# Kernel tuning notes

Hardware: AMD Instinct MI355X
Metric: run time of the kernel (lower is better)

The kernel has to match this reference:

```python
import jax, jax.numpy as jnp
import numpy as np

NEG = -1.0e4  # neg_limit sentinel used for masked max-pool (fp16-safe)

def setup_inputs() -> dict:
    B, S, H, MW = 4, 2048, 768, 8
    N = S * MW  # num_spans = seq_len * max_span_width
    key = jax.random.key(0)
    k1, k2, k3, k4, k5 = jax.random.split(key, 5)
    token_reps = jax.random.normal(k1, (B, S, H), dtype=jnp.float32)
    starts = jax.random.randint(k2, (B, N), 0, S)
    widths = jax.random.randint(k3, (B, N), 1, MW + 1)
    ends = jnp.minimum(starts + widths, S)  # end-exclusive, <= seq_len
    span_ids = jnp.stack([starts, ends], axis=-1).astype(jnp.int64)
    span_masks = jax.random.uniform(k4, (B, N)) < 0.7
    # ProjectionLayer(2*hidden -> hidden): linear reprojection (dropout inactive at eval)
    W = jax.random.normal(k5, (2 * H, H), dtype=jnp.float32) * 0.02
    b = jnp.zeros((H,), dtype=jnp.float32)
    return {"token_reps": token_reps, "span_ids": span_ids, "span_masks": span_masks,
            "pooling": 0, "W": W, "b": b}

def _window_max(token_reps, idx, valid):
    # idx, valid: (B, N, w); gather tokens then masked max over the window
    B, S, H = token_reps.shape
    w = idx.shape[-1]
    idxc = jnp.clip(idx, 0, S - 1).reshape(B, -1, 1)          # (B, N*w, 1)
    g = jnp.take_along_axis(token_reps, idxc, axis=1)          # (B, N*w, H)
    g = g.reshape(B, -1, w, H)                                 # (B, N, w, H)
    g = jnp.where(valid[..., None], g, NEG)
    return g.max(axis=2)                                       # (B, N, H)

def reference(token_reps, span_ids, span_masks, pooling, W, b):
    # Faithful to extract_span_reps(mode='start_end') but via direct gather+max
    # over the fixed window instead of a (B,N,S,H) broadcasted mask.
    window = 1 if pooling else 3
    starts = span_ids[..., 0]
    ends = span_ids[..., 1]
    offs = jnp.arange(window)
    # start window: [start, min(start+window, end))
    s_idx = starts[..., None] + offs                                   # (B,N,w)
    s_valid = (s_idx < ends[..., None]) & span_masks[..., None]
    # end window: [max(end-window, start), end)
    e_idx = ends[..., None] - window + offs                            # (B,N,w)
    e_valid = (e_idx >= starts[..., None]) & span_masks[..., None]
    start_reps = _window_max(token_reps, s_idx, s_valid)
    end_reps = _window_max(token_reps, e_idx, e_valid)
    span_reps = jnp.concatenate([start_reps, end_reps], axis=-1)       # (B,N,2H)
    span_reps = jnp.where(span_masks[..., None], span_reps, 0.0)
    # out_project: Linear(2H -> H)
    return jnp.einsum('bnd,dh->bnh', span_reps, W) + b
```

## Files before the change

kernel.cpp:

```cpp
#include <hip/hip_runtime.h>
#include <hip/hip_bf16.h>

#define NB 4
#define SEQ 2048
#define HID 768
#define NSPAN 16384
#define M_TOT (NB * NSPAN)
#define K2 1536
#define MROWS (NB * 3 * SEQ)
#define CMP_CAP 66560
#define MT_TOT 520
#define NWG_OLD (MT_TOT * 6)
#define NWG_NEW 2304

typedef float f32x4 __attribute__((ext_vector_type(4)));
typedef short s16x8 __attribute__((ext_vector_type(8)));
typedef unsigned short u16x4 __attribute__((ext_vector_type(4)));
using bf16 = __hip_bfloat16;

__device__ __forceinline__ void gll16(const void* g, void* l) {
    __builtin_amdgcn_global_load_lds(
        (const __attribute__((address_space(1))) unsigned*)g,
        (__attribute__((address_space(3))) unsigned*)l, 16, 0, 0);
}

__device__ __forceinline__ float bf2f(unsigned short v) {
    union { unsigned u; float f; } cv; cv.u = ((unsigned)v) << 16; return cv.f;
}

__global__ void mask_detect_kernel(const unsigned* __restrict__ masks, int* __restrict__ flag) {
    int t = blockIdx.x * 256 + threadIdx.x;
    if (t < 16384) {
        unsigned v = masks[t];
        if (v > 1u) atomicOr(flag, 1);
    }
}

__device__ __forceinline__ bool mask_at(const int* masks, int u8, int m) {
    return u8 ? (((const unsigned char*)masks)[m] != 0) : (masks[m] != 0);
}

__global__ void prep_m3_kernel(const float* __restrict__ T, bf16* __restrict__ M3) {
    int b = blockIdx.y;
    int p0 = blockIdx.x * 16;
    int t = threadIdx.x;
    const float* Tb = T + (size_t)b * SEQ * HID;
    bf16* o0 = M3 + (size_t)(b * 3 + 0) * SEQ * HID;
    bf16* o1 = M3 + (size_t)(b * 3 + 1) * SEQ * HID;
    bf16* o2 = M3 + (size_t)(b * 3 + 2) * SEQ * HID;
#pragma unroll
    for (int c = 0; c < 3; ++c) {
        int h = t + c * 256;
        float x0 = Tb[(size_t)p0 * HID + h];
        float x1 = Tb[(size_t)min(p0 + 1, SEQ - 1) * HID + h];
        for (int i = 0; i < 16; ++i) {
            int p = p0 + i;
            float x2 = Tb[(size_t)min(p + 2, SEQ - 1) * HID + h];
            float m2 = fmaxf(x0, x1);
            float m3v = fmaxf(m2, x2);
            size_t off = (size_t)p * HID + h;
            o0[off] = __float2bfloat16(x0);
            o1[off] = __float2bfloat16(m2);
            o2[off] = __float2bfloat16(m3v);
            x0 = x1; x1 = x2;
        }
    }
}


__global__ void prep_wt2_kernel(const float* __restrict__ W, bf16* __restrict__ Wt) {
    __shared__ float tile[64][65];
    int k0 = blockIdx.x * 64;
    int n0 = blockIdx.y * 64;
    int half = (n0 >= HID) ? 1 : 0;
    int nn = n0 - half * HID;
    int t = threadIdx.x;
    int c = t & 63, r4 = t >> 6;
    for (int r = r4; r < 64; r += 4)
        tile[r][c] = W[(size_t)(half * HID + k0 + r) * HID + nn + c];
    __syncthreads();
    for (int r = r4; r < 64; r += 4)
        Wt[(size_t)(n0 + r) * HID + k0 + c] = __float2bfloat16(tile[c][r]);
}

__global__ __launch_bounds__(256, 4)
void dense_gemm_kernel(const bf16* __restrict__ M3, const bf16* __restrict__ Wt,
                       bf16* __restrict__ P) {
    __shared__ char lA[16384];
    __shared__ char lB[16384];

    const int tid = threadIdx.x;
    const int x = blockIdx.x;
    const int g = x & 7, j = x >> 3;
    const int mt = (j / 12) * 8 + g;
    const int ns = j % 12;
    const int m0 = mt * 128, n0 = ns * 128;

    const int lane = tid & 63, w = tid >> 6;
    const int wr = w >> 1, wc = w & 1;
    const int lr = lane & 15, lg = lane >> 4;
    const int lrow8 = lane >> 3;
    const int chunkp = ((lane & 7) ^ lrow8) << 4;

    const char* aPtr[4];
    const char* bPtr[4];
    int ldsOff[4];
#pragma unroll
    for (int it = 0; it < 4; ++it) {
        int i = it * 4 + w;
        int r = i * 8 + lrow8;
        aPtr[it] = (const char*)M3 + (size_t)(m0 + r) * (HID * 2) + chunkp;
        bPtr[it] = (const char*)Wt + (size_t)(n0 + r) * (HID * 2) + chunkp;
        ldsOff[it] = i * 1024;
    }

    f32x4 acc[4][4];
#pragma unroll
    for (int i = 0; i < 4; i++)
#pragma unroll
        for (int j2 = 0; j2 < 4; j2++) acc[i][j2] = (f32x4){0.f, 0.f, 0.f, 0.f};

    for (int kt = 0; kt < HID; kt += 64) {
        const int colB = kt * 2;
        __syncthreads();
#pragma unroll
        for (int it = 0; it < 4; ++it)
            gll16(aPtr[it] + colB, lA + ldsOff[it]);
#pragma unroll
        for (int it = 0; it < 4; ++it)
            gll16(bPtr[it] + colB, lB + ldsOff[it]);
        __syncthreads();
#pragma unroll
        for (int kk = 0; kk < 2; ++kk) {
            const int cb = kk * 4 + lg;
            s16x8 af[4], bfr[4];
#pragma unroll
            for (int i = 0; i < 4; ++i) {
                int row = wr * 64 + i * 16 + lr;
                af[i] = *(const s16x8*)(lA + row * 128 + ((cb ^ (row & 7)) << 4));
            }
#pragma unroll
            for (int j2 = 0; j2 < 4; ++j2) {
                int row = wc * 64 + j2 * 16 + lr;
                bfr[j2] = *(const s16x8*)(lB + row * 128 + ((cb ^ (row & 7)) << 4));
            }
#pragma unroll
            for (int i = 0; i < 4; ++i)
#pragma unroll
                for (int j2 = 0; j2 < 4; ++j2)
                    acc[i][j2] = __builtin_amdgcn_mfma_f32_16x16x32_bf16(af[i], bfr[j2], acc[i][j2], 0, 0, 0);
        }
    }

    unsigned short* Pu = (unsigned short*)P;
#pragma unroll
    for (int i = 0; i < 4; i++) {
#pragma unroll
        for (int j2 = 0; j2 < 4; j2++) {
#pragma unroll
            for (int q = 0; q < 4; q++) {
                int prow = m0 + wr * 64 + i * 16 + lg * 4 + q;
                int pcol = n0 + wc * 64 + j2 * 16 + lr;
                bf16 v = __float2bfloat16(acc[i][j2][q]);
                Pu[(size_t)prow * K2 + pcol] = *(unsigned short*)&v;
            }
        }
    }
}

__global__ __launch_bounds__(256)
void epilogue_kernel(const bf16* __restrict__ P, const int* __restrict__ span_ids,
                     const int* __restrict__ masks, const int* __restrict__ flag,
                     const int* __restrict__ pooling, const float* __restrict__ bias,
                     float* __restrict__ out) {
    int gw = (blockIdx.x * 256 + threadIdx.x) >> 6;
    int lane = threadIdx.x & 63;
    int u8 = flag[0];
    int window = (pooling[0] != 0) ? 1 : 3;
    const unsigned short* Pu = (const unsigned short*)P;
    for (int m = gw; m < M_TOT; m += 8192) {
        float* orow = out + (size_t)m * HID;
        if (!mask_at(masks, u8, m)) {
#pragma unroll
            for (int rnd = 0; rnd < 3; ++rnd) {
                int n = rnd * 256 + lane * 4;
                *(f32x4*)(orow + n) = *(const f32x4*)(bias + n);
            }
            continue;
        }
        int s = span_ids[2 * m], e = span_ids[2 * m + 1];
        int b = m >> 14;
        int cw = min(window, e - s);
        int base = (b * 3 + (cw - 1)) * SEQ;
        const unsigned short* ps = Pu + (size_t)(base + s) * K2;
        const unsigned short* pe = Pu + (size_t)(base + e - cw) * K2 + HID;
#pragma unroll
        for (int rnd = 0; rnd < 3; ++rnd) {
            int n = rnd * 256 + lane * 4;
            u16x4 a = *(const u16x4*)(ps + n);
            u16x4 c = *(const u16x4*)(pe + n);
            f32x4 bb = *(const f32x4*)(bias + n);
            f32x4 r;
#pragma unroll
            for (int k = 0; k < 4; ++k) r[k] = bf2f(a[k]) + bf2f(c[k]) + bb[k];
            *(f32x4*)(orow + n) = r;
        }
    }
}


__global__ void init_compact_kernel(int* __restrict__ cS, int* __restrict__ cE,
                                    int* __restrict__ cO) {
    int i = blockIdx.x * 256 + threadIdx.x;
    if (i < CMP_CAP) { cS[i] = 0; cE[i] = 0; cO[i] = -1; }
}

__global__ void count_kernel(const int* __restrict__ masks, const int* __restrict__ flag,
                             int* __restrict__ blockCnt) {
    int bid = blockIdx.x, tid = threadIdx.x;
    bool act = mask_at(masks, flag[0], bid * 256 + tid);
    unsigned long long b = __ballot(act);
    __shared__ int wc[4];
    if ((tid & 63) == 0) wc[tid >> 6] = __popcll(b);
    __syncthreads();
    if (tid == 0) blockCnt[bid] = wc[0] + wc[1] + wc[2] + wc[3];
}

__global__ void scan_kernel(const int* __restrict__ blockCnt, int* __restrict__ blockOff,
                            int* __restrict__ cnt) {
    __shared__ int s[256];
    int t = threadIdx.x;
    int mine = blockCnt[t];
    s[t] = mine;
    __syncthreads();
    for (int d = 1; d < 256; d <<= 1) {
        int v = (t >= d) ? s[t - d] : 0;
        __syncthreads();
        s[t] += v;
        __syncthreads();
    }
    blockOff[t] = s[t] - mine;
    if (t == 255) cnt[0] = s[255];
}

__global__ void scatter_kernel(const int* __restrict__ span_ids, const int* __restrict__ masks,
                               const int* __restrict__ flag, const int* __restrict__ pooling,
                               const int* __restrict__ blockOff,
                               int* __restrict__ cS, int* __restrict__ cE,
                               int* __restrict__ cO, int* __restrict__ cI) {
    int bid = blockIdx.x, tid = threadIdx.x;
    int m = bid * 256 + tid;
    bool act = mask_at(masks, flag[0], m);
    unsigned long long b = __ballot(act);
    __shared__ int wA[4], wI[4];
    int lane = tid & 63, w = tid >> 6;
    int wAct = __popcll(b);
    if (lane == 0) { wA[w] = wAct; wI[w] = 64 - wAct; }
    __syncthreads();
    if (tid == 0) {
        int a = 0, ii = 0;
#pragma unroll
        for (int i = 0; i < 4; ++i) {
            int ca = wA[i], ci = wI[i];
            wA[i] = a; wI[i] = ii; a += ca; ii += ci;
        }
    }
    __syncthreads();
    unsigned long long below = (lane == 63) ? ~0ULL >> 1 : ((1ULL << lane) - 1ULL);
    if (act) {
        int rank = __popcll(b & below);
        int idx = blockOff[bid] + wA[w] + rank;
        int s = span_ids[2 * m], e = span_ids[2 * m + 1];
        int bb = m >> 14;
        int window = (pooling[0] != 0) ? 1 : 3;
        int cw = min(window, e - s);
        int base = (bb * 3 + (cw - 1)) * SEQ;
        cS[idx] = base + s;
        cE[idx] = base + (e - cw);
        cO[idx] = m;
    } else {
        int rank = __popcll(~b & below);
        int idx = (bid * 256 - blockOff[bid]) + wI[w] + rank;
        cI[idx] = m;
    }
}

__global__ void prep_wt_old_kernel(const float* __restrict__ W, bf16* __restrict__ Wt) {
    __shared__ float tile[64][65];
    int k0 = blockIdx.x * 64;
    int n0 = blockIdx.y * 64;
    int t = threadIdx.x;
    int c = t & 63, r4 = t >> 6;
    for (int r = r4; r < 64; r += 4)
        tile[r][c] = W[(size_t)(k0 + r) * HID + n0 + c];
    __syncthreads();
    for (int r = r4; r < 64; r += 4)
        Wt[(size_t)(n0 + r) * K2 + k0 + c] = __float2bfloat16(tile[c][r]);
}

__global__ __launch_bounds__(256, 4)
void span_gemm_old_kernel(const bf16* __restrict__ M3, const bf16* __restrict__ Wt,
                          const int* __restrict__ cS, const int* __restrict__ cE,
                          const int* __restrict__ cO, const int* __restrict__ cI,
                          const int* __restrict__ cnt,
                          const float* __restrict__ bias, float* __restrict__ out) {
    __shared__ char lA[128 * 128];
    __shared__ char lB[128 * 128];
    __shared__ int rS[128], rE[128], rO[128];

    const int tid = threadIdx.x;
    const int x = blockIdx.x;
    const int g = x & 7, j = x >> 3;
    const int mt = (j / 6) * 8 + g;
    const int ns = j % 6;
    const int n0 = ns * 128;

    const int count = cnt[0];
    const int actT = (count + 127) >> 7;

    if (mt >= actT) {
        int r = (mt - actT) * 128 + (tid >> 1);
        if (r < M_TOT - count) {
            int o = cI[r];
            const float* bsrc = bias + n0 + (tid & 1) * 64;
            float* dst = out + (size_t)o * HID + n0 + (tid & 1) * 64;
#pragma unroll
            for (int c = 0; c < 16; ++c)
                *(f32x4*)(dst + c * 4) = *(const f32x4*)(bsrc + c * 4);
        }
        return;
    }

    const int m0 = mt * 128;
    if (tid < 128) {
        int m = m0 + tid;
        rS[tid] = cS[m];
        rE[tid] = cE[m];
        rO[tid] = cO[m];
    }
    __syncthreads();

    const int lane = tid & 63, w = tid >> 6;
    const int wr = w >> 1, wc = w & 1;
    const int lr = lane & 15, lg = lane >> 4;
    const int lrow8 = lane >> 3;
    const int chunkp = ((lane & 7) ^ lrow8) << 4;

    const char* aPtr[2][4];
    const char* bPtr[4];
    int ldsOff[4];
#pragma unroll
    for (int it = 0; it < 4; ++it) {
        int i = it * 4 + w;
        int r = i * 8 + lrow8;
        aPtr[0][it] = (const char*)M3 + (size_t)rS[r] * (HID * 2) + chunkp;
        aPtr[1][it] = (const char*)M3 + (size_t)rE[r] * (HID * 2) + chunkp;
        bPtr[it]    = (const char*)Wt + (size_t)(n0 + r) * (K2 * 2) + chunkp;
        ldsOff[it]  = i * 1024;
    }

    f32x4 acc[4][4];
#pragma unroll
    for (int i = 0; i < 4; i++)
#pragma unroll
        for (int j2 = 0; j2 < 4; j2++) acc[i][j2] = (f32x4){0.f, 0.f, 0.f, 0.f};

    for (int kt = 0; kt < K2; kt += 64) {
        const int half = (kt >= HID) ? 1 : 0;
        const int colB = (kt - (half ? HID : 0)) * 2;
        const int ktB  = kt * 2;
        __syncthreads();
#pragma unroll
        for (int it = 0; it < 4; ++it)
            gll16(aPtr[half][it] + colB, lA + ldsOff[it]);
#pragma unroll
        for (int it = 0; it < 4; ++it)
            gll16(bPtr[it] + ktB, lB + ldsOff[it]);
        __syncthreads();
#pragma unroll
        for (int kk = 0; kk < 2; ++kk) {
            const int cb = kk * 4 + lg;
            s16x8 af[4], bfr[4];
#pragma unroll
            for (int i = 0; i < 4; ++i) {
                int row = wr * 64 + i * 16 + lr;
                af[i] = *(const s16x8*)(lA + row * 128 + ((cb ^ (row & 7)) << 4));
            }
#pragma unroll
            for (int j2 = 0; j2 < 4; ++j2) {
                int row = wc * 64 + j2 * 16 + lr;
                bfr[j2] = *(const s16x8*)(lB + row * 128 + ((cb ^ (row & 7)) << 4));
            }
#pragma unroll
            for (int i = 0; i < 4; ++i)
#pragma unroll
                for (int j2 = 0; j2 < 4; ++j2)
                    acc[i][j2] = __builtin_amdgcn_mfma_f32_16x16x32_bf16(af[i], bfr[j2], acc[i][j2], 0, 0, 0);
        }
    }

#pragma unroll
    for (int i = 0; i < 4; i++) {
#pragma unroll
        for (int j2 = 0; j2 < 4; j2++) {
#pragma unroll
            for (int q = 0; q < 4; q++) {
                int mloc = wr * 64 + i * 16 + lg * 4 + q;
                int o = rO[mloc];
                if (o >= 0) {
                    int n = n0 + wc * 64 + j2 * 16 + lr;
                    out[(size_t)o * HID + n] = acc[i][j2][q] + bias[n];
                }
            }
        }
    }
}

extern "C" void kernel_launch(void* const* d_in, const int* in_sizes, int n_in,
                              void* d_out, int out_size, void* d_ws, size_t ws_size,
                              hipStream_t stream) {
    const float* token_reps = (const float*)d_in[0];
    const int*   span_ids   = (const int*)d_in[1];
    const int*   span_masks = (const int*)d_in[2];
    const int*   pooling    = (const int*)d_in[3];
    const float* W          = (const float*)d_in[4];
    const float* bias       = (const float*)d_in[5];
    float* out = (float*)d_out;

    char* ws = (char*)d_ws;
    int*  flag = (int*)ws;

    const size_t M3_OFF   = (size_t)2 << 20;
    const size_t M3_BYTES = (size_t)MROWS * HID * 2;
    bf16* M3 = (bf16*)(ws + M3_OFF);

    const size_t WT2_OFF  = M3_OFF + M3_BYTES;
    const size_t WT2_BYTES = (size_t)K2 * HID * 2;
    const size_t P_OFF    = WT2_OFF + WT2_BYTES;
    const size_t P_BYTES  = (size_t)MROWS * K2 * 2;
    const size_t NEED_NEW = P_OFF + P_BYTES;

    hipMemsetAsync(ws, 0, 64, stream);
    mask_detect_kernel<<<64, 256, 0, stream>>>((const unsigned*)span_masks, flag);
    prep_m3_kernel<<<dim3(SEQ / 16, NB), 256, 0, stream>>>(token_reps, M3);

    if (ws_size >= NEED_NEW) {
        bf16* Wt2 = (bf16*)(ws + WT2_OFF);
        bf16* P   = (bf16*)(ws + P_OFF);
        prep_wt2_kernel<<<dim3(HID / 64, K2 / 64), 256, 0, stream>>>(W, Wt2);
        dense_gemm_kernel<<<NWG_NEW, 256, 0, stream>>>(M3, Wt2, P);
        epilogue_kernel<<<2048, 256, 0, stream>>>(P, span_ids, span_masks, flag,
                                                  pooling, bias, out);
    } else {
        int* cnt      = (int*)(ws + 4);
        int* blockCnt = (int*)(ws + 1024);
        int* blockOff = (int*)(ws + 2048);
        int* cS = (int*)(ws + 4096);
        int* cE = (int*)(ws + 4096 + 4 * (size_t)CMP_CAP);
        int* cO = (int*)(ws + 4096 + 8 * (size_t)CMP_CAP);
        int* cI = (int*)(ws + 4096 + 12 * (size_t)CMP_CAP);
        bf16* WtOld = (bf16*)(ws + WT2_OFF);
        init_compact_kernel<<<(CMP_CAP + 255) / 256, 256, 0, stream>>>(cS, cE, cO);
        count_kernel<<<M_TOT / 256, 256, 0, stream>>>(span_masks, flag, blockCnt);
        scan_kernel<<<1, 256, 0, stream>>>(blockCnt, blockOff, cnt);
        scatter_kernel<<<M_TOT / 256, 256, 0, stream>>>(span_ids, span_masks, flag,
                                                        pooling, blockOff, cS, cE, cO, cI);
        prep_wt_old_kernel<<<dim3(K2 / 64, HID / 64), 256, 0, stream>>>(W, WtOld);
        span_gemm_old_kernel<<<NWG_OLD, 256, 0, stream>>>(
            M3, WtOld, cS, cE, cO, cI, cnt, bias, out);
    }
}
```

Before: 149.7 us.

## Restructure dense GEMM into 256x128 tiles with 512 threads and multi-buffered async LDS pipeline

Measured after the change: 159.9 us. 1.07x slower.

```diff
diff --git a/kernel.cpp b/kernel.cpp
--- a/kernel.cpp
+++ b/kernel.cpp
@@ -8,10 +8,11 @@
 #define M_TOT (NB * NSPAN)
 #define K2 1536
 #define MROWS (NB * 3 * SEQ)
+#define NT12 12
 #define CMP_CAP 66560
 #define MT_TOT 520
 #define NWG_OLD (MT_TOT * 6)
-#define NWG_NEW 2304
+#define NWG_NEW 1152
 
 typedef float f32x4 __attribute__((ext_vector_type(4)));
 typedef short s16x8 __attribute__((ext_vector_type(8)));
@@ -83,36 +84,45 @@
         Wt[(size_t)(n0 + r) * HID + k0 + c] = __float2bfloat16(tile[c][r]);
 }
 
-__global__ __launch_bounds__(256, 4)
+__global__ __launch_bounds__(512, 1)
 void dense_gemm_kernel(const bf16* __restrict__ M3, const bf16* __restrict__ Wt,
                        bf16* __restrict__ P) {
-    __shared__ char lA[16384];
-    __shared__ char lB[16384];
+    __shared__ char lds[131072];
 
     const int tid = threadIdx.x;
     const int x = blockIdx.x;
     const int g = x & 7, j = x >> 3;
     const int mt = (j / 12) * 8 + g;
     const int ns = j % 12;
-    const int m0 = mt * 128, n0 = ns * 128;
+    const int m0 = mt * 256, n0 = ns * 128;
 
     const int lane = tid & 63, w = tid >> 6;
-    const int wr = w >> 1, wc = w & 1;
+    const int wm = w >> 1, wn = w & 1;
     const int lr = lane & 15, lg = lane >> 4;
-    const int lrow8 = lane >> 3;
-    const int chunkp = ((lane & 7) ^ lrow8) << 4;
-
-    const char* aPtr[4];
-    const char* bPtr[4];
-    int ldsOff[4];
-#pragma unroll
-    for (int it = 0; it < 4; ++it) {
-        int i = it * 4 + w;
-        int r = i * 8 + lrow8;
-        aPtr[it] = (const char*)M3 + (size_t)(m0 + r) * (HID * 2) + chunkp;
-        bPtr[it] = (const char*)Wt + (size_t)(n0 + r) * (HID * 2) + chunkp;
-        ldsOff[it] = i * 1024;
-    }
+
+    const int srow_w = w * 8 + (lane >> 3);
+    const int swz = ((lane & 7) ^ ((lane >> 3) & 7)) << 4;
+    const char* aSrc[4];
+    const char* bSrc[2];
+#pragma unroll
+    for (int q = 0; q < 4; ++q)
+        aSrc[q] = (const char*)M3 + (size_t)(m0 + q * 64 + srow_w) * (HID * 2) + swz;
+#pragma unroll
+    for (int q = 0; q < 2; ++q)
+        bSrc[q] = (const char*)Wt + (size_t)(n0 + q * 64 + srow_w) * (HID * 2) + swz;
+    const int dstOff = w * 1024;
+
+#define ST_A(T) do { char* _b = lds + ((T) % 3) * 32768; const int _c = (T) * 128; \
+        gll16(aSrc[0] + _c, _b + 0 * 8192 + dstOff); \
+        gll16(aSrc[1] + _c, _b + 1 * 8192 + dstOff); \
+        gll16(aSrc[2] + _c, _b + 2 * 8192 + dstOff); \
+        gll16(aSrc[3] + _c, _b + 3 * 8192 + dstOff); } while (0)
+#define ST_B(T) do { char* _b = lds + 98304 + ((T) & 1) * 16384; const int _c = (T) * 128; \
+        gll16(bSrc[0] + _c, _b + 0 * 8192 + dstOff); \
+        gll16(bSrc[1] + _c, _b + 1 * 8192 + dstOff); } while (0)
+#define FENCE_BAR() do { __builtin_amdgcn_sched_barrier(0); \
+        __builtin_amdgcn_s_barrier(); \
+        __builtin_amdgcn_sched_barrier(0); } while (0)
 
     f32x4 acc[4][4];
 #pragma unroll
@@ -120,37 +130,69 @@
 #pragma unroll
         for (int j2 = 0; j2 < 4; j2++) acc[i][j2] = (f32x4){0.f, 0.f, 0.f, 0.f};
 
-    for (int kt = 0; kt < HID; kt += 64) {
-        const int colB = kt * 2;
-        __syncthreads();
-#pragma unroll
-        for (int it = 0; it < 4; ++it)
-            gll16(aPtr[it] + colB, lA + ldsOff[it]);
-#pragma unroll
-        for (int it = 0; it < 4; ++it)
-            gll16(bPtr[it] + colB, lB + ldsOff[it]);
-        __syncthreads();
-#pragma unroll
-        for (int kk = 0; kk < 2; ++kk) {
-            const int cb = kk * 4 + lg;
-            s16x8 af[4], bfr[4];
-#pragma unroll
-            for (int i = 0; i < 4; ++i) {
-                int row = wr * 64 + i * 16 + lr;
-                af[i] = *(const s16x8*)(lA + row * 128 + ((cb ^ (row & 7)) << 4));
-            }
-#pragma unroll
-            for (int j2 = 0; j2 < 4; ++j2) {
-                int row = wc * 64 + j2 * 16 + lr;
-                bfr[j2] = *(const s16x8*)(lB + row * 128 + ((cb ^ (row & 7)) << 4));
-            }
-#pragma unroll
-            for (int i = 0; i < 4; ++i)
-#pragma unroll
-                for (int j2 = 0; j2 < 4; ++j2)
-                    acc[i][j2] = __builtin_amdgcn_mfma_f32_16x16x32_bf16(af[i], bfr[j2], acc[i][j2], 0, 0, 0);
-        }
-    }
+    ST_A(0); ST_B(0); ST_A(1); ST_B(1);
+
+    for (int t = 0; t < NT12; ++t) {
+        const char* Ab = lds + (t % 3) * 32768;
+        const char* Bb = lds + 98304 + (t & 1) * 16384;
+        s16x8 bfr[4][2];
+
+        if (t < NT12 - 1) { asm volatile("s_waitcnt vmcnt(6)" ::: "memory"); }
+        else              { asm volatile("s_waitcnt vmcnt(0)" ::: "memory"); }
+        FENCE_BAR();
+        if (t + 2 < NT12) ST_A(t + 2);
+#pragma unroll
+        for (int jf = 0; jf < 4; ++jf) {
+            int row = wn * 64 + jf * 16 + lr;
+#pragma unroll
+            for (int ks = 0; ks < 2; ++ks)
+                bfr[jf][ks] = *(const s16x8*)(Bb + row * 128 + ((((ks << 2) | lg) ^ (row & 7)) << 4));
+        }
+        {
+            s16x8 af[2][2];
+#pragma unroll
+            for (int i = 0; i < 2; ++i) {
+                int row = wm * 64 + i * 16 + lr;
+#pragma unroll
+                for (int ks = 0; ks < 2; ++ks)
+                    af[i][ks] = *(const s16x8*)(Ab + row * 128 + ((((ks << 2) | lg) ^ (row & 7)) << 4));
+            }
+            __builtin_amdgcn_s_setprio(1);
+#pragma unroll
+            for (int ks = 0; ks < 2; ++ks)
+#pragma unroll
+                for (int i = 0; i < 2; ++i)
+#pragma unroll
+                    for (int jf = 0; jf < 4; ++jf)
+                        acc[i][jf] = __builtin_amdgcn_mfma_f32_16x16x32_bf16(af[i][ks], bfr[jf][ks], acc[i][jf], 0, 0, 0);
+            __builtin_amdgcn_s_setprio(0);
+        }
+
+        FENCE_BAR();
+        if (t + 2 < NT12) ST_B(t + 2);
+        {
+            s16x8 af[2][2];
+#pragma unroll
+            for (int i = 0; i < 2; ++i) {
+                int row = wm * 64 + (i + 2) * 16 + lr;
+#pragma unroll
+                for (int ks = 0; ks < 2; ++ks)
+                    af[i][ks] = *(const s16x8*)(Ab + row * 128 + ((((ks << 2) | lg) ^ (row & 7)) << 4));
+            }
+            __builtin_amdgcn_s_setprio(1);
+#pragma unroll
+            for (int ks = 0; ks < 2; ++ks)
+#pragma unroll
+                for (int i = 0; i < 2; ++i)
+#pragma unroll
+                    for (int jf = 0; jf < 4; ++jf)
+                        acc[i + 2][jf] = __builtin_amdgcn_mfma_f32_16x16x32_bf16(af[i][ks], bfr[jf][ks], acc[i + 2][jf], 0, 0, 0);
+            __builtin_amdgcn_s_setprio(0);
+        }
+    }
+#undef ST_A
+#undef ST_B
+#undef FENCE_BAR
 
     unsigned short* Pu = (unsigned short*)P;
 #pragma unroll
@@ -159,8 +201,8 @@
         for (int j2 = 0; j2 < 4; j2++) {
 #pragma unroll
             for (int q = 0; q < 4; q++) {
-                int prow = m0 + wr * 64 + i * 16 + lg * 4 + q;
-                int pcol = n0 + wc * 64 + j2 * 16 + lr;
+                int prow = m0 + wm * 64 + i * 16 + lg * 4 + q;
+                int pcol = n0 + wn * 64 + j2 * 16 + lr;
                 bf16 v = __float2bfloat16(acc[i][j2][q]);
                 Pu[(size_t)prow * K2 + pcol] = *(unsigned short*)&v;
             }
@@ -448,7 +490,7 @@
         bf16* Wt2 = (bf16*)(ws + WT2_OFF);
         bf16* P   = (bf16*)(ws + P_OFF);
         prep_wt2_kernel<<<dim3(HID / 64, K2 / 64), 256, 0, stream>>>(W, Wt2);
-        dense_gemm_kernel<<<NWG_NEW, 256, 0, stream>>>(M3, Wt2, P);
+        dense_gemm_kernel<<<NWG_NEW, 512, 0, stream>>>(M3, Wt2, P);
         epilogue_kernel<<<2048, 256, 0, stream>>>(P, span_ids, span_masks, flag,
                                                   pooling, bias, out);
     } else {
```
